# Kernel optimization log

Hardware: AMD Instinct MI355X
Metric: run time of the kernel (lower is better)

Reference implementation:

```python
import jax, jax.numpy as jnp
import numpy as np

N = 100000   # nodes ('paper')
E = 500000   # edges per etype
ET = 3       # edge types
L = 2        # GAT layers
F = 256      # in_feats == h_feats
H = 4        # heads
D = 64       # head dim = h_feats // n_heads
C = 349      # num_classes
NEG_SLOPE = 0.2


def setup_inputs() -> dict:
    key = jax.random.key(0)
    ks = jax.random.split(key, 10)
    x = jax.random.normal(ks[0], (N, F), jnp.float32)
    # stacked per-(layer, etype) GATConv params
    W = jax.random.normal(ks[1], (L, ET, F, H * D), jnp.float32) * 0.05
    attn_l = jax.random.normal(ks[2], (L, ET, H, D), jnp.float32) * 0.1
    attn_r = jax.random.normal(ks[3], (L, ET, H, D), jnp.float32) * 0.1
    bias = jnp.zeros((L, ET, H * D), jnp.float32)
    W_out = jax.random.normal(ks[4], (H * D, C), jnp.float32) * 0.05
    b_out = jnp.zeros((C,), jnp.float32)
    src = jax.random.randint(ks[5], (ET, E), 0, N, dtype=jnp.int32)
    dst = jax.random.randint(ks[6], (ET, E), 0, N, dtype=jnp.int32)
    return {"x": x, "W": W, "attn_l": attn_l, "attn_r": attn_r, "bias": bias,
            "W_out": W_out, "b_out": b_out, "src": src, "dst": dst}


def _gat_etype(h, W_le, al, ar, b, s, d):
    # h: [N,F] -> feat: [N,H,D]
    feat = (h @ W_le).reshape(-1, H, D)
    el = jnp.einsum('nhd,hd->nh', feat, al)   # [N,H]
    er = jnp.einsum('nhd,hd->nh', feat, ar)   # [N,H]
    logits = jax.nn.leaky_relu(el[s] + er[d], NEG_SLOPE)  # [E,H]
    # segment softmax over incoming edges of each dst node
    m = jax.ops.segment_max(logits, d, num_segments=N)     # [N,H]
    a = jnp.exp(logits - m[d])                              # [E,H]
    denom = jax.ops.segment_sum(a, d, num_segments=N)      # [N,H]
    alpha = a / denom[d]                                    # [E,H]
    msg = alpha[:, :, None] * feat[s]                       # [E,H,D]
    agg = jax.ops.segment_sum(msg, d, num_segments=N)      # [N,H,D]
    return agg + b.reshape(H, D)


def reference(x, W, attn_l, attn_r, bias, W_out, b_out, src, dst):
    h = x
    for l in range(L):
        out = jnp.zeros((N, H, D), x.dtype)
        for e in range(ET):  # HeteroGraphConv default 'sum' aggregation
            out = out + _gat_etype(h, W[l, e], attn_l[l, e], attn_r[l, e],
                                   bias[l, e], src[e], dst[e])
        h = out.reshape(N, H * D)  # concat heads (view)
        if l != L - 1:
            h = jax.nn.relu(h)  # dropout is identity in eval mode
    return h @ W_out + b_out
```

## Files before the change

### kernel.cpp

```cpp
#include <hip/hip_runtime.h>
#include <hip/hip_fp16.h>

#define N_NODES 100000
#define N_EDGES 500000
#define M_PAD   100096
#define N3      300000
#define NPB     512
#define NBUK    196
#define KEYS_B  1536
#define BCAP    12288
#define CH_A    8192
#define NBLK_A  184

using f32x4  = __attribute__((ext_vector_type(4))) float;
using bf16x8 = __attribute__((ext_vector_type(8))) __bf16;

__device__ __forceinline__ ushort f2bf(float f) {
  union { float f; unsigned u; } v; v.f = f;
  unsigned r = v.u + 0x7fffu + ((v.u >> 16) & 1u);
  return (ushort)(r >> 16);
}
__device__ __forceinline__ float bf2f(ushort b) {
  union { unsigned u; float f; } v; v.u = ((unsigned)b) << 16;
  return v.f;
}

__global__ __launch_bounds__(256) void cvt_x_kernel(const float* __restrict__ x,
                                                    ushort* __restrict__ h) {
  const size_t i = (size_t)blockIdx.x * 256 + threadIdx.x;
  ushort4 o;
  if (i < (size_t)N_NODES * 64) {
    const float4 v = ((const float4*)x)[i];
    o.x = f2bf(v.x); o.y = f2bf(v.y); o.z = f2bf(v.z); o.w = f2bf(v.w);
  } else {
    o.x = 0; o.y = 0; o.z = 0; o.w = 0;
  }
  ((ushort4*)h)[i] = o;
}

__global__ __launch_bounds__(256) void cvt_w_kernel(const float* __restrict__ W,
                                                    ushort* __restrict__ Wt) {
  const int i = blockIdx.x * 256 + threadIdx.x;
  const int le = i >> 16, r = i & 65535, nn = r >> 8, kk = r & 255;
  Wt[i] = f2bf(W[(le << 16) | (kk << 8) | nn]);
}

__global__ __launch_bounds__(256) void cvt_wout_kernel(const float* __restrict__ Wo,
                                                       ushort* __restrict__ Wto) {
  const int i = blockIdx.x * 256 + threadIdx.x;
  const int nn = i >> 8, kk = i & 255;
  Wto[i] = f2bf(nn < 349 ? Wo[kk * 349 + nn] : 0.f);
}

__global__ __launch_bounds__(256) void zero_gcnt_kernel(int* __restrict__ gcnt) {
  const int i = threadIdx.x;
  if (i < NBUK) gcnt[i] = 0;
}

__global__ __launch_bounds__(256) void bucketA_kernel(const int* __restrict__ src,
                                                      const int* __restrict__ dst,
                                                      int* __restrict__ gcnt,
                                                      uint* __restrict__ barr) {
  __shared__ int cnt[NBUK];
  __shared__ int ofs[NBUK];
  const int t = threadIdx.x;
  const int base = blockIdx.x * CH_A;
  const int lim = (3 * N_EDGES - base < CH_A) ? (3 * N_EDGES - base) : CH_A;
  for (int b = t; b < NBUK; b += 256) cnt[b] = 0;
  __syncthreads();
  for (int k = t; k < lim; k += 256) {
    const int d = dst[base + k];
    atomicAdd(&cnt[d >> 9], 1);
  }
  __syncthreads();
  if (t < NBUK) {
    ofs[t] = atomicAdd(&gcnt[t], cnt[t]);
    cnt[t] = 0;
  }
  __syncthreads();
  for (int k = t; k < lim; k += 256) {
    const int i = base + k;
    const int d = dst[i];
    const int et = (i >= 2 * N_EDGES) ? 2 : ((i >= N_EDGES) ? 1 : 0);
    const uint key = (uint)((d & (NPB - 1)) * 3 + et);
    const uint sid = (uint)(et * M_PAD + src[i]);
    const int buk = d >> 9;
    int pos = ofs[buk] + atomicAdd(&cnt[buk], 1);
    if (pos < BCAP)
      barr[(size_t)buk * BCAP + pos] = (key << 19) | sid;
  }
}

__global__ __launch_bounds__(256) void scan196_kernel(const int* __restrict__ gcnt,
                                                      int* __restrict__ bbase,
                                                      int* __restrict__ rowp3) {
  __shared__ int sm[256];
  const int t = threadIdx.x;
  const int v = (t < NBUK) ? gcnt[t] : 0;
  sm[t] = v; __syncthreads();
  for (int off = 1; off < 256; off <<= 1) {
    const int x = (t >= off) ? sm[t - off] : 0;
    __syncthreads();
    sm[t] += x;
    __syncthreads();
  }
  if (t < NBUK) bbase[t] = sm[t] - v;
  if (t == 0) rowp3[N3] = 3 * N_EDGES;
}

__global__ __launch_bounds__(256) void csrB_kernel(const uint* __restrict__ barr,
                                                   const int* __restrict__ gcnt,
                                                   const int* __restrict__ bbase,
                                                   int* __restrict__ rowp3,
                                                   uint* __restrict__ srcid) {
  __shared__ int hist[KEYS_B];
  __shared__ int excl[KEYS_B];
  __shared__ int tsum[256];
  const int b = blockIdx.x, t = threadIdx.x;
  const int n = gcnt[b] < BCAP ? gcnt[b] : BCAP;
  const int cbase = bbase[b];
  const uint* ba = barr + (size_t)b * BCAP;
  for (int k = t; k < KEYS_B; k += 256) hist[k] = 0;
  __syncthreads();
  for (int r = t; r < n; r += 256) atomicAdd(&hist[ba[r] >> 19], 1);
  __syncthreads();
  int loc[6];
  int s = 0;
#pragma unroll
  for (int j = 0; j < 6; ++j) { loc[j] = s; s += hist[t * 6 + j]; }
  tsum[t] = s; __syncthreads();
  for (int off = 1; off < 256; off <<= 1) {
    const int x = (t >= off) ? tsum[t - off] : 0;
    __syncthreads();
    tsum[t] += x;
    __syncthreads();
  }
  const int tbase = tsum[t] - s;
#pragma unroll
  for (int j = 0; j < 6; ++j) excl[t * 6 + j] = tbase + loc[j];
  __syncthreads();
  const int nrem = (N_NODES - b * NPB) * 3;
  const int kmax = (nrem < KEYS_B) ? nrem : KEYS_B;
  for (int k = t; k < KEYS_B; k += 256) {
    if (k < kmax) rowp3[b * KEYS_B + k] = cbase + excl[k];
    hist[k] = 0;
  }
  __syncthreads();
  for (int r = t; r < n; r += 256) {
    const uint rec = ba[r];
    const int key = (int)(rec >> 19);
    const int pos = excl[key] + atomicAdd(&hist[key], 1);
    srcid[cbase + pos] = rec & 0x7FFFFu;
  }
}

__global__ __launch_bounds__(256, 2) void gemm_feat_fused(
    const ushort* __restrict__ A, const ushort* __restrict__ WtL,
    ushort* __restrict__ feat, const float* __restrict__ attn_l,
    const float* __restrict__ attn_r, float* __restrict__ el,
    float* __restrict__ er, int layer) {
  __shared__ ushort As[128 * 64];
  __shared__ ushort Bs[3 * 128 * 64];
  const int t = threadIdx.x;
  const int lane = t & 63;
  const int wave = t >> 6;
  const int wm = (wave >> 1) << 6;
  const int wn = (wave & 1) << 6;
  const int quad = lane >> 4;
  const int ln = lane & 15;
  const size_t m0 = (size_t)blockIdx.x * 128;
  const size_t n0 = (size_t)blockIdx.y * 128;

  f32x4 acc[3][4][4];
#pragma unroll
  for (int e = 0; e < 3; ++e)
#pragma unroll
    for (int x = 0; x < 4; ++x)
#pragma unroll
      for (int y = 0; y < 4; ++y)
        acc[e][x][y] = (f32x4){0.f, 0.f, 0.f, 0.f};

  for (int k0 = 0; k0 < 256; k0 += 64) {
    __syncthreads();
#pragma unroll
    for (int i = 0; i < 4; ++i) {
      const int f = i * 256 + t;
      const int row = f >> 3;
      const int cl = (f & 7) ^ (row & 7);
      const int ldsbase = (i * 256 + (t & ~63)) << 3;
      __builtin_amdgcn_global_load_lds(
          (const __attribute__((address_space(1))) void*)(A + (m0 + row) * 256 + k0 + cl * 8),
          (__attribute__((address_space(3))) void*)(As + ldsbase), 16, 0, 0);
#pragma unroll
      for (int e = 0; e < 3; ++e)
        __builtin_amdgcn_global_load_lds(
            (const __attribute__((address_space(1))) void*)(WtL + (e << 16) + (n0 + row) * 256 + k0 + cl * 8),
            (__attribute__((address_space(3))) void*)(Bs + e * 8192 + ldsbase), 16, 0, 0);
    }
    __syncthreads();
#pragma unroll
    for (int s = 0; s < 2; ++s) {
      const int cl = s * 4 + quad;
      bf16x8 af[4];
#pragma unroll
      for (int x = 0; x < 4; ++x) {
        const int mm = wm + x * 16 + ln;
        af[x] = *(const bf16x8*)(As + mm * 64 + ((cl ^ (mm & 7)) << 3));
      }
#pragma unroll
      for (int e = 0; e < 3; ++e) {
        bf16x8 bfr[4];
#pragma unroll
        for (int y = 0; y < 4; ++y) {
          const int nn = wn + y * 16 + ln;
          bfr[y] = *(const bf16x8*)(Bs + e * 8192 + nn * 64 + ((cl ^ (nn & 7)) << 3));
        }
#pragma unroll
        for (int x = 0; x < 4; ++x)
#pragma unroll
          for (int y = 0; y < 4; ++y)
            acc[e][x][y] = __builtin_amdgcn_mfma_f32_16x16x32_bf16(bfr[y], af[x], acc[e][x][y], 0, 0, 0);
      }
    }
  }

  const int h = (int)(n0 + wn) >> 6;
#pragma unroll
  for (int e = 0; e < 3; ++e) {
    ushort* C = feat + (size_t)e * M_PAD * 256;
#pragma unroll
    for (int x = 0; x < 4; ++x) {
      const size_t m = m0 + wm + x * 16 + ln;
#pragma unroll
      for (int y = 0; y < 4; ++y) {
        const size_t n = n0 + wn + y * 16 + quad * 4;
        ushort4 o;
        o.x = f2bf(acc[e][x][y][0]); o.y = f2bf(acc[e][x][y][1]);
        o.z = f2bf(acc[e][x][y][2]); o.w = f2bf(acc[e][x][y][3]);
        *(ushort4*)(C + m * 256 + n) = o;
      }
    }
    const float* al = attn_l + (((layer * 3 + e) * 4 + h) << 6);
    const float* ar = attn_r + (((layer * 3 + e) * 4 + h) << 6);
    float4 alv[4], arv[4];
#pragma unroll
    for (int y = 0; y < 4; ++y) {
      alv[y] = *(const float4*)(al + y * 16 + quad * 4);
      arv[y] = *(const float4*)(ar + y * 16 + quad * 4);
    }
#pragma unroll
    for (int x = 0; x < 4; ++x) {
      float pl = 0.f, pr = 0.f;
#pragma unroll
      for (int y = 0; y < 4; ++y) {
        pl += acc[e][x][y][0] * alv[y].x + acc[e][x][y][1] * alv[y].y +
              acc[e][x][y][2] * alv[y].z + acc[e][x][y][3] * alv[y].w;
        pr += acc[e][x][y][0] * arv[y].x + acc[e][x][y][1] * arv[y].y +
              acc[e][x][y][2] * arv[y].z + acc[e][x][y][3] * arv[y].w;
      }
      pl += __shfl_xor(pl, 16); pl += __shfl_xor(pl, 32);
      pr += __shfl_xor(pr, 16); pr += __shfl_xor(pr, 32);
      const int m = (int)m0 + wm + x * 16 + ln;
      if (quad == 0 && m < N_NODES) {
        el[((size_t)e * M_PAD + m) * 4 + h] = pl;
        er[((size_t)e * M_PAD + m) * 4 + h] = pr;
      }
    }
  }
}

__global__ __launch_bounds__(256) void gemm128(const ushort* __restrict__ A,
                                               const ushort* __restrict__ Bt,
                                               float* __restrict__ C,
                                               const float* __restrict__ obias,
                                               int ldc, int nmax, int mmax) {
  __shared__ ushort As[128 * 64];
  __shared__ ushort Bs[128 * 64];
  const int t = threadIdx.x;
  const int lane = t & 63;
  const int wave = t >> 6;
  const int wm = (wave >> 1) << 6;
  const int wn = (wave & 1) << 6;
  const int quad = lane >> 4;
  const int ln = lane & 15;
  const size_t m0 = (size_t)blockIdx.x * 128;
  const size_t n0 = (size_t)blockIdx.y * 128;

  f32x4 acc[4][4];
#pragma unroll
  for (int x = 0; x < 4; ++x)
#pragma unroll
    for (int y = 0; y < 4; ++y)
      acc[x][y] = (f32x4){0.f, 0.f, 0.f, 0.f};

  for (int k0 = 0; k0 < 256; k0 += 64) {
    __syncthreads();
#pragma unroll
    for (int i = 0; i < 4; ++i) {
      const int f = i * 256 + t;
      const int row = f >> 3;
      const int cl = (f & 7) ^ (row & 7);
      const int ldsbase = (i * 256 + (t & ~63)) << 3;
      __builtin_amdgcn_global_load_lds(
          (const __attribute__((address_space(1))) void*)(A + (m0 + row) * 256 + k0 + cl * 8),
          (__attribute__((address_space(3))) void*)(As + ldsbase), 16, 0, 0);
      __builtin_amdgcn_global_load_lds(
          (const __attribute__((address_space(1))) void*)(Bt + (n0 + row) * 256 + k0 + cl * 8),
          (__attribute__((address_space(3))) void*)(Bs + ldsbase), 16, 0, 0);
    }
    __syncthreads();
#pragma unroll
    for (int s = 0; s < 2; ++s) {
      bf16x8 af[4], bfr[4];
      const int cl = s * 4 + quad;
#pragma unroll
      for (int x = 0; x < 4; ++x) {
        const int mm = wm + x * 16 + ln;
        af[x] = *(const bf16x8*)(As + mm * 64 + ((cl ^ (mm & 7)) << 3));
        const int nn = wn + x * 16 + ln;
        bfr[x] = *(const bf16x8*)(Bs + nn * 64 + ((cl ^ (nn & 7)) << 3));
      }
#pragma unroll
      for (int x = 0; x < 4; ++x)
#pragma unroll
        for (int y = 0; y < 4; ++y)
          acc[x][y] = __builtin_amdgcn_mfma_f32_16x16x32_bf16(bfr[y], af[x], acc[x][y], 0, 0, 0);
    }
  }

#pragma unroll
  for (int x = 0; x < 4; ++x) {
    const int m = (int)m0 + wm + x * 16 + ln;
    if (m < mmax) {
#pragma unroll
      for (int y = 0; y < 4; ++y) {
        const int n = (int)n0 + wn + y * 16 + quad * 4;
#pragma unroll
        for (int r = 0; r < 4; ++r)
          if (n + r < nmax)
            C[(size_t)m * ldc + n + r] = acc[x][y][r] + obias[n + r];
      }
    }
  }
}

__global__ __launch_bounds__(256) void wden_kernel(const int* __restrict__ rowp3,
                                                   const uint* __restrict__ srcid,
                                                   const float* __restrict__ el,
                                                   const float* __restrict__ er,
                                                   ushort* __restrict__ wcsr) {
  const int wv   = __builtin_amdgcn_readfirstlane((int)(threadIdx.x >> 6));
  const int lane = threadIdx.x & 63;
  const int h    = lane & 3;
  const int eo   = lane >> 2;
  for (int n = blockIdx.x * 4 + wv; n < N_NODES; n += 8192) {
#pragma unroll
    for (int et = 0; et < 3; ++et) {
      const int b = rowp3[n * 3 + et];
      const int e = rowp3[n * 3 + et + 1];
      const int deg = e - b;
      if (deg == 0) continue;
      const float erh = er[(((size_t)et * M_PAD + n) << 2) + h];
      if (deg <= 16) {
        const int idx = b + eo;
        const bool valid = idx < e;
        const uint sid = srcid[valid ? idx : b];
        float z = el[((size_t)sid << 2) + h] + erh;
        z = (z > 0.f) ? z : 0.2f * z;
        const float w = valid ? __expf(z) : 0.f;
        float s = w;
        s += __shfl_xor(s, 4);  s += __shfl_xor(s, 8);
        s += __shfl_xor(s, 16); s += __shfl_xor(s, 32);
        const float r = __builtin_amdgcn_rcpf(s);
        if (valid)
          wcsr[((size_t)idx << 2) + h] = __half_as_ushort(__float2half(w * r));
      } else {
        float s = 0.f;
        for (int i0 = b; i0 < e; i0 += 16) {
          const int idx = i0 + eo;
          const bool valid = idx < e;
          const uint sid = srcid[valid ? idx : b];
          float z = el[((size_t)sid << 2) + h] + erh;
          z = (z > 0.f) ? z : 0.2f * z;
          const float w = valid ? __expf(z) : 0.f;
          if (valid)
            wcsr[((size_t)idx << 2) + h] = __half_as_ushort(__float2half(w));
          s += w;
        }
        s += __shfl_xor(s, 4);  s += __shfl_xor(s, 8);
        s += __shfl_xor(s, 16); s += __shfl_xor(s, 32);
        const float r = __builtin_amdgcn_rcpf(s);
        for (int i0 = b; i0 < e; i0 += 16) {
          const int idx = i0 + eo;
          if (idx < e) {
            const float w = __half2float(__ushort_as_half(wcsr[((size_t)idx << 2) + h]));
            wcsr[((size_t)idx << 2) + h] = __half_as_ushort(__float2half(w * r));
          }
        }
      }
    }
  }
}

__global__ __launch_bounds__(256) void agg_kernel(const ushort* __restrict__ feat,
                                                  const ushort* __restrict__ wcsr,
                                                  const int* __restrict__ rowp3,
                                                  const uint* __restrict__ srcid,
                                                  const float* __restrict__ bias,
                                                  ushort* __restrict__ hout,
                                                  int layer, int do_relu) {
  const int wv   = __builtin_amdgcn_readfirstlane((int)(threadIdx.x >> 6));
  const int lane = threadIdx.x & 63;
  const int h2   = (lane >> 4) << 1;
  const int f8   = lane << 3;
  const float* bl = bias + layer * 768 + (lane << 2);
  const float b0 = bl[0] + bl[256] + bl[512];
  const float b1 = bl[1] + bl[257] + bl[513];
  const float b2 = bl[2] + bl[258] + bl[514];
  const float b3 = bl[3] + bl[259] + bl[515];
  const char* wb = (const char*)wcsr;
  const char* fb = (const char*)feat;
  for (int n = blockIdx.x * 4 + wv; n < N_NODES; n += 8192) {
    const int beg = rowp3[n * 3];
    const int end = rowp3[n * 3 + 3];
    float a0 = b0, a1 = b1, a2 = b2, a3 = b3;
    if (end > beg) {
      const int last = end - 1;
      float l0 = 0.f, l1 = 0.f, l2 = 0.f, l3 = 0.f;
      for (int i = beg; i < end; i += 8) {
        int idx[8];
#pragma unroll
        for (int j = 0; j < 8; ++j)
          idx[j] = (i + j < last) ? (i + j) : last;
        uint sd[8];
#pragma unroll
        for (int j = 0; j < 8; ++j)
          sd[j] = srcid[idx[j]];
        float wj[8];
#pragma unroll
        for (int j = 0; j < 8; ++j) {
          const ushort wu = *(const ushort*)(wb + ((size_t)idx[j] << 3) + h2);
          const float t = __half2float(__ushort_as_half(wu));
          wj[j] = (i + j <= last) ? t : 0.f;
        }
        uint2 fv[8];
#pragma unroll
        for (int j = 0; j < 8; ++j)
          fv[j] = *(const uint2*)(fb + ((size_t)sd[j] << 9) + f8);
#pragma unroll
        for (int j = 0; j < 8; ++j) {
          union { uint u; float f; } c0, c1, c2, c3;
          c0.u = fv[j].x << 16;
          c1.u = fv[j].x & 0xffff0000u;
          c2.u = fv[j].y << 16;
          c3.u = fv[j].y & 0xffff0000u;
          l0 += wj[j] * c0.f;
          l1 += wj[j] * c1.f;
          l2 += wj[j] * c2.f;
          l3 += wj[j] * c3.f;
        }
      }
      a0 += l0; a1 += l1; a2 += l2; a3 += l3;
    }
    if (do_relu) {
      a0 = fmaxf(a0, 0.f); a1 = fmaxf(a1, 0.f);
      a2 = fmaxf(a2, 0.f); a3 = fmaxf(a3, 0.f);
    }
    ushort4 o;
    o.x = f2bf(a0); o.y = f2bf(a1); o.z = f2bf(a2); o.w = f2bf(a3);
    *(ushort4*)(hout + (size_t)n * 256 + (lane << 2)) = o;
  }
}

extern "C" void kernel_launch(void* const* d_in, const int* in_sizes, int n_in,
                              void* d_out, int out_size, void* d_ws, size_t ws_size,
                              hipStream_t stream) {
  const float* x      = (const float*)d_in[0];
  const float* W      = (const float*)d_in[1];
  const float* attn_l = (const float*)d_in[2];
  const float* attn_r = (const float*)d_in[3];
  const float* bias   = (const float*)d_in[4];
  const float* W_out  = (const float*)d_in[5];
  const float* b_out  = (const float*)d_in[6];
  const int*   src    = (const int*)d_in[7];
  const int*   dst    = (const int*)d_in[8];

  char* p = (char*)d_ws;
  auto carve = [&](size_t bytes) {
    char* r = p;
    p += (bytes + 255) & ~(size_t)255;
    return r;
  };
  ushort* h_bf  = (ushort*)carve((size_t)M_PAD * 256 * 2);
  ushort* feat  = (ushort*)carve((size_t)3 * M_PAD * 256 * 2);
  ushort* Wt    = (ushort*)carve((size_t)6 * 65536 * 2);
  ushort* Wto   = (ushort*)carve((size_t)384 * 256 * 2);
  float*  el    = (float*)carve((size_t)3 * M_PAD * 4 * 4);
  float*  er    = (float*)carve((size_t)3 * M_PAD * 4 * 4);
  int*    rowp3 = (int*)carve((size_t)(N3 + 1) * 4);
  uint*   srcid = (uint*)carve((size_t)3 * N_EDGES * 4);
  ushort* wcsr  = (ushort*)carve((size_t)3 * N_EDGES * 4 * 2);
  uint*   barr  = (uint*)carve((size_t)NBUK * BCAP * 4);
  int*    gcnt  = (int*)carve((size_t)NBUK * 4);
  int*    bbase = (int*)carve((size_t)NBUK * 4);

  cvt_x_kernel<<<M_PAD * 64 / 256, 256, 0, stream>>>(x, h_bf);
  cvt_w_kernel<<<6 * 65536 / 256, 256, 0, stream>>>(W, Wt);
  cvt_wout_kernel<<<384 * 256 / 256, 256, 0, stream>>>(W_out, Wto);

  zero_gcnt_kernel<<<1, 256, 0, stream>>>(gcnt);
  bucketA_kernel<<<NBLK_A, 256, 0, stream>>>(src, dst, gcnt, barr);
  scan196_kernel<<<1, 256, 0, stream>>>(gcnt, bbase, rowp3);
  csrB_kernel<<<NBUK, 256, 0, stream>>>(barr, gcnt, bbase, rowp3, srcid);

  for (int l = 0; l < 2; ++l) {
    gemm_feat_fused<<<dim3(M_PAD / 128, 2), 256, 0, stream>>>(
        h_bf, Wt + (size_t)l * 3 * 65536, feat, attn_l, attn_r, el, er, l);
    wden_kernel<<<2048, 256, 0, stream>>>(rowp3, srcid, el, er, wcsr);
    agg_kernel<<<2048, 256, 0, stream>>>(feat, wcsr, rowp3, srcid, bias,
                                         h_bf, l, l == 0 ? 1 : 0);
  }
  gemm128<<<dim3(M_PAD / 128, 3), 256, 0, stream>>>(h_bf, Wto, (float*)d_out,
                                                    b_out, 349, 349, N_NODES);
}
```

Before: 867.3 us.

## Fuse edge softmax into aggregation and balance waves by edge count

Removes the separate wden kernel that wrote normalized fp16 attention weights to memory. The aggregation kernel now computes exp(leaky_relu(el+er)) per edge on the fly, keeps a running denominator, and normalizes once per edge type. A new bounds kernel binary-searches the CSR row pointer so each wave gets a contiguous node range with roughly equal edge counts, replacing the strided node-per-wave loop. The trade-offs are exp work duplicated across the 16 lanes of each head, and the loss of max subtraction, which relies on small logits to avoid overflow.

```diff
diff --git a/kernel.cpp b/kernel.cpp
--- a/kernel.cpp
+++ b/kernel.cpp
@@ -11,6 +11,7 @@
 #define BCAP    12288
 #define CH_A    8192
 #define NBLK_A  184
+#define NWAVES  8192
 
 using f32x4  = __attribute__((ext_vector_type(4))) float;
 using bf16x8 = __attribute__((ext_vector_type(8))) __bf16;
@@ -152,6 +153,21 @@
     const int pos = excl[key] + atomicAdd(&hist[key], 1);
     srcid[cbase + pos] = rec & 0x7FFFFu;
   }
+}
+
+__global__ __launch_bounds__(256) void bounds_kernel(const int* __restrict__ rowp3,
+                                                     int* __restrict__ wbeg) {
+  const int w = blockIdx.x * 256 + threadIdx.x;
+  if (w > NWAVES) return;
+  if (w == 0)      { wbeg[0] = 0;            return; }
+  if (w == NWAVES) { wbeg[NWAVES] = N_NODES; return; }
+  const int target = (int)(((long long)w * (3LL * N_EDGES)) >> 13);
+  int lo = 0, hi = N_NODES;
+  while (lo < hi) {
+    const int mid = (lo + hi) >> 1;
+    if (rowp3[mid * 3] < target) lo = mid + 1; else hi = mid;
+  }
+  wbeg[w] = lo;
 }
 
 __global__ __launch_bounds__(256, 2) void gemm_feat_fused(
@@ -344,90 +360,39 @@
   }
 }
 
-__global__ __launch_bounds__(256) void wden_kernel(const int* __restrict__ rowp3,
-                                                   const uint* __restrict__ srcid,
-                                                   const float* __restrict__ el,
-                                                   const float* __restrict__ er,
-                                                   ushort* __restrict__ wcsr) {
-  const int wv   = __builtin_amdgcn_readfirstlane((int)(threadIdx.x >> 6));
-  const int lane = threadIdx.x & 63;
-  const int h    = lane & 3;
-  const int eo   = lane >> 2;
-  for (int n = blockIdx.x * 4 + wv; n < N_NODES; n += 8192) {
-#pragma unroll
-    for (int et = 0; et < 3; ++et) {
-      const int b = rowp3[n * 3 + et];
-      const int e = rowp3[n * 3 + et + 1];
-      const int deg = e - b;
-      if (deg == 0) continue;
-      const float erh = er[(((size_t)et * M_PAD + n) << 2) + h];
-      if (deg <= 16) {
-        const int idx = b + eo;
-        const bool valid = idx < e;
-        const uint sid = srcid[valid ? idx : b];
-        float z = el[((size_t)sid << 2) + h] + erh;
-        z = (z > 0.f) ? z : 0.2f * z;
-        const float w = valid ? __expf(z) : 0.f;
-        float s = w;
-        s += __shfl_xor(s, 4);  s += __shfl_xor(s, 8);
-        s += __shfl_xor(s, 16); s += __shfl_xor(s, 32);
-        const float r = __builtin_amdgcn_rcpf(s);
-        if (valid)
-          wcsr[((size_t)idx << 2) + h] = __half_as_ushort(__float2half(w * r));
-      } else {
-        float s = 0.f;
-        for (int i0 = b; i0 < e; i0 += 16) {
-          const int idx = i0 + eo;
-          const bool valid = idx < e;
-          const uint sid = srcid[valid ? idx : b];
-          float z = el[((size_t)sid << 2) + h] + erh;
-          z = (z > 0.f) ? z : 0.2f * z;
-          const float w = valid ? __expf(z) : 0.f;
-          if (valid)
-            wcsr[((size_t)idx << 2) + h] = __half_as_ushort(__float2half(w));
-          s += w;
-        }
-        s += __shfl_xor(s, 4);  s += __shfl_xor(s, 8);
-        s += __shfl_xor(s, 16); s += __shfl_xor(s, 32);
-        const float r = __builtin_amdgcn_rcpf(s);
-        for (int i0 = b; i0 < e; i0 += 16) {
-          const int idx = i0 + eo;
-          if (idx < e) {
-            const float w = __half2float(__ushort_as_half(wcsr[((size_t)idx << 2) + h]));
-            wcsr[((size_t)idx << 2) + h] = __half_as_ushort(__float2half(w * r));
-          }
-        }
-      }
-    }
-  }
-}
-
 __global__ __launch_bounds__(256) void agg_kernel(const ushort* __restrict__ feat,
-                                                  const ushort* __restrict__ wcsr,
                                                   const int* __restrict__ rowp3,
                                                   const uint* __restrict__ srcid,
+                                                  const float* __restrict__ el,
+                                                  const float* __restrict__ er,
                                                   const float* __restrict__ bias,
+                                                  const int* __restrict__ wbeg,
                                                   ushort* __restrict__ hout,
                                                   int layer, int do_relu) {
-  const int wv   = __builtin_amdgcn_readfirstlane((int)(threadIdx.x >> 6));
+  const int wid  = __builtin_amdgcn_readfirstlane(
+                     (int)(blockIdx.x * 4 + (threadIdx.x >> 6)));
   const int lane = threadIdx.x & 63;
-  const int h2   = (lane >> 4) << 1;
+  const int quad = lane >> 4;
   const int f8   = lane << 3;
   const float* bl = bias + layer * 768 + (lane << 2);
   const float b0 = bl[0] + bl[256] + bl[512];
   const float b1 = bl[1] + bl[257] + bl[513];
   const float b2 = bl[2] + bl[258] + bl[514];
   const float b3 = bl[3] + bl[259] + bl[515];
-  const char* wb = (const char*)wcsr;
   const char* fb = (const char*)feat;
-  for (int n = blockIdx.x * 4 + wv; n < N_NODES; n += 8192) {
-    const int beg = rowp3[n * 3];
-    const int end = rowp3[n * 3 + 3];
+  const int nbeg = wbeg[wid];
+  const int nend = wbeg[wid + 1];
+  for (int n = nbeg; n < nend; ++n) {
     float a0 = b0, a1 = b1, a2 = b2, a3 = b3;
-    if (end > beg) {
-      const int last = end - 1;
-      float l0 = 0.f, l1 = 0.f, l2 = 0.f, l3 = 0.f;
-      for (int i = beg; i < end; i += 8) {
+#pragma unroll
+    for (int et = 0; et < 3; ++et) {
+      const int b = rowp3[n * 3 + et];
+      const int e = rowp3[n * 3 + et + 1];
+      if (e == b) continue;
+      const float erh = er[(((size_t)et * M_PAD + n) << 2) + quad];
+      const int last = e - 1;
+      float l0 = 0.f, l1 = 0.f, l2 = 0.f, l3 = 0.f, den = 0.f;
+      for (int i = b; i < e; i += 8) {
         int idx[8];
 #pragma unroll
         for (int j = 0; j < 8; ++j)
@@ -436,17 +401,21 @@
 #pragma unroll
         for (int j = 0; j < 8; ++j)
           sd[j] = srcid[idx[j]];
-        float wj[8];
-#pragma unroll
-        for (int j = 0; j < 8; ++j) {
-          const ushort wu = *(const ushort*)(wb + ((size_t)idx[j] << 3) + h2);
-          const float t = __half2float(__ushort_as_half(wu));
-          wj[j] = (i + j <= last) ? t : 0.f;
-        }
+        float zl[8];
+#pragma unroll
+        for (int j = 0; j < 8; ++j)
+          zl[j] = el[((size_t)sd[j] << 2) + quad];
         uint2 fv[8];
 #pragma unroll
         for (int j = 0; j < 8; ++j)
           fv[j] = *(const uint2*)(fb + ((size_t)sd[j] << 9) + f8);
+        float wj[8];
+#pragma unroll
+        for (int j = 0; j < 8; ++j) {
+          float z = zl[j] + erh;
+          z = (z > 0.f) ? z : 0.2f * z;
+          wj[j] = (i + j <= last) ? __expf(z) : 0.f;
+        }
 #pragma unroll
         for (int j = 0; j < 8; ++j) {
           union { uint u; float f; } c0, c1, c2, c3;
@@ -454,13 +423,15 @@
           c1.u = fv[j].x & 0xffff0000u;
           c2.u = fv[j].y << 16;
           c3.u = fv[j].y & 0xffff0000u;
+          den += wj[j];
           l0 += wj[j] * c0.f;
           l1 += wj[j] * c1.f;
           l2 += wj[j] * c2.f;
           l3 += wj[j] * c3.f;
         }
       }
-      a0 += l0; a1 += l1; a2 += l2; a3 += l3;
+      const float inv = __builtin_amdgcn_rcpf(den);
+      a0 += l0 * inv; a1 += l1 * inv; a2 += l2 * inv; a3 += l3 * inv;
     }
     if (do_relu) {
       a0 = fmaxf(a0, 0.f); a1 = fmaxf(a1, 0.f);
@@ -499,10 +470,10 @@
   float*  er    = (float*)carve((size_t)3 * M_PAD * 4 * 4);
   int*    rowp3 = (int*)carve((size_t)(N3 + 1) * 4);
   uint*   srcid = (uint*)carve((size_t)3 * N_EDGES * 4);
-  ushort* wcsr  = (ushort*)carve((size_t)3 * N_EDGES * 4 * 2);
   uint*   barr  = (uint*)carve((size_t)NBUK * BCAP * 4);
   int*    gcnt  = (int*)carve((size_t)NBUK * 4);
   int*    bbase = (int*)carve((size_t)NBUK * 4);
+  int*    wbeg  = (int*)carve((size_t)(NWAVES + 1) * 4);
 
   cvt_x_kernel<<<M_PAD * 64 / 256, 256, 0, stream>>>(x, h_bf);
   cvt_w_kernel<<<6 * 65536 / 256, 256, 0, stream>>>(W, Wt);
@@ -512,13 +483,13 @@
   bucketA_kernel<<<NBLK_A, 256, 0, stream>>>(src, dst, gcnt, barr);
   scan196_kernel<<<1, 256, 0, stream>>>(gcnt, bbase, rowp3);
   csrB_kernel<<<NBUK, 256, 0, stream>>>(barr, gcnt, bbase, rowp3, srcid);
+  bounds_kernel<<<(NWAVES + 256) / 256, 256, 0, stream>>>(rowp3, wbeg);
 
   for (int l = 0; l < 2; ++l) {
     gemm_feat_fused<<<dim3(M_PAD / 128, 2), 256, 0, stream>>>(
         h_bf, Wt + (size_t)l * 3 * 65536, feat, attn_l, attn_r, el, er, l);
-    wden_kernel<<<2048, 256, 0, stream>>>(rowp3, srcid, el, er, wcsr);
-    agg_kernel<<<2048, 256, 0, stream>>>(feat, wcsr, rowp3, srcid, bias,
-                                         h_bf, l, l == 0 ? 1 : 0);
+    agg_kernel<<<2048, 256, 0, stream>>>(feat, rowp3, srcid, el, er, bias,
+                                         wbeg, h_bf, l, l == 0 ? 1 : 0);
   }
   gemm128<<<dim3(M_PAD / 128, 3), 256, 0, stream>>>(h_bf, Wto, (float*)d_out,
                                                     b_out, 349, 349, N_NODES);
```

Measured after the change: 964.2 us. 11.2% more time.
